# Kernel optimization log

Hardware: AMD Instinct MI355X
Metric: run time of the kernel (lower is better)

The kernel has to match this reference:

```python
import jax, jax.numpy as jnp
import numpy as np

V, E, H, L, C, NH, O, B = 32000, 128, 128, 6, 4, 4, 1024, 16384
HD = H // NH


def setup_inputs() -> dict:
    key = jax.random.key(0)
    ks = jax.random.split(key, 20)
    s = 1.0 / np.sqrt(H).astype(np.float32)

    def rn(k, shape, scale=s):
        return jax.random.normal(k, shape, jnp.float32) * scale

    return {
        "tokens": jax.random.randint(ks[0], (B, 1), 0, V),
        "h": jax.random.normal(ks[1], (L, C, B, H), jnp.float32),
        "emb": rn(ks[2], (V, E), 1.0),
        "wih0_c0": rn(ks[3], (3 * H, E)),
        "wih0_rest": rn(ks[4], (C - 1, 3 * H, 1)),
        "bih0": rn(ks[5], (C, 3 * H)),
        "whh0": rn(ks[6], (C, 3 * H, H)),
        "bhh0": rn(ks[7], (C, 3 * H)),
        "wih": rn(ks[8], (L - 1, C, 3 * H, H)),
        "whh": rn(ks[9], (L - 1, C, 3 * H, H)),
        "bih": rn(ks[10], (L - 1, C, 3 * H)),
        "bhh": rn(ks[11], (L - 1, C, 3 * H)),
        "attn_in_w": rn(ks[12], (L, 3 * H, H)),
        "attn_in_b": rn(ks[13], (L, 3 * H)),
        "attn_out_w": rn(ks[14], (L, H, H), 0.001),  # nn.init.normal_(out_proj.weight, 0, 0.001)
        "attn_out_b": jnp.zeros((L, H), jnp.float32),
        "ln_g": jnp.ones((L, H), jnp.float32),
        "ln_b": jnp.zeros((L, H), jnp.float32),
        "gate_w": rn(ks[15], (L, 2 * H)),
        "gate_b": jnp.zeros((L,), jnp.float32),
        "head_w": rn(ks[16], (O, H)),
        "head_b": jnp.zeros((O,), jnp.float32),
    }


def _gru(gi, gh, h):
    # torch GRUCell: r,z gates sigmoid; n = tanh(in + r*hn); h' = (1-z)*n + z*h
    ir, iz, i_n = jnp.split(gi, 3, -1)
    hr, hz, h_n = jnp.split(gh, 3, -1)
    r = jax.nn.sigmoid(ir + hr)
    z = jax.nn.sigmoid(iz + hz)
    n = jnp.tanh(i_n + r * h_n)
    return (1.0 - z) * n + z * h


def _msg_layer(hn, in_w, in_b, out_w, out_b, g, b):
    # hn: [C,B,H]; MultiheadAttention with batch_first=False (seq=C), then LayerNorm
    qkv = jnp.einsum('cbh,gh->cbg', hn, in_w) + in_b
    q, k, v = jnp.split(qkv, 3, -1)
    q = q.reshape(C, -1, NH, HD)
    k = k.reshape(C, -1, NH, HD)
    v = v.reshape(C, -1, NH, HD)
    scores = jnp.einsum('qbnd,kbnd->bnqk', q, k) / np.sqrt(HD).astype(np.float32)
    a = jax.nn.softmax(scores, axis=-1)
    o = jnp.einsum('bnqk,kbnd->qbnd', a, v).reshape(C, -1, H)
    o = jnp.einsum('cbh,oh->cbo', o, out_w) + out_b
    mu = o.mean(-1, keepdims=True)
    var = o.var(-1, keepdims=True)
    return (o - mu) / jnp.sqrt(var + 1e-5) * g + b


def reference(tokens, h, emb, wih0_c0, wih0_rest, bih0, whh0, bhh0, wih, whh, bih, bhh,
              attn_in_w, attn_in_b, attn_out_w, attn_out_b, ln_g, ln_b,
              gate_w, gate_b, head_w, head_b):
    bsz = tokens.shape[0]
    x0 = emb[tokens[:, 0]]  # [B,E]
    x = None
    h_new = []
    for l in range(L):
        hl = h[l]  # [C,B,H]
        if l == 0:
            gi0 = x0 @ wih0_c0.T + bih0[0]  # col 0 gets the embedding
            # cols 1..C-1 get a zeros(B,1) dummy input -> x @ wih0_rest == 0, bias only
            gi_rest = jnp.broadcast_to(bih0[1:, None, :], (C - 1, bsz, 3 * H))
            gi = jnp.concatenate([gi0[None], gi_rest], 0)
            whh_l, bhh_l = whh0, bhh0
        else:
            gi = jnp.einsum('cbi,cgi->cbg', x, wih[l - 1]) + bih[l - 1][:, None, :]
            whh_l, bhh_l = whh[l - 1], bhh[l - 1]
        gh = jnp.einsum('cbi,cgi->cbg', hl, whh_l) + bhh_l[:, None, :]
        hl_n = _gru(gi, gh, hl)
        msg = _msg_layer(hl_n, attn_in_w[l], attn_in_b[l], attn_out_w[l], attn_out_b[l], ln_g[l], ln_b[l])
        gin = jnp.concatenate([hl_n, msg], -1)  # [C,B,2H]
        gt = jax.nn.sigmoid(jnp.einsum('cbh,h->cb', gin, gate_w[l]) + gate_b[l])[..., None]
        hl_n = (1.0 - gt) * hl_n + gt * msg
        h_new.append(hl_n)
        x = hl_n
    h_n = jnp.stack(h_new, 0)  # [L,C,B,H]
    y = h_n[-1, 0] @ head_w.T + head_b  # head on last layer, column 0
    return (y, h_n)
```

## Files before the change

### kernel.cpp

```cpp
#include <hip/hip_runtime.h>
#include <hip/hip_bf16.h>

#define B_   16384
#define H_   128
#define C_   4
#define L_   6
#define O_   1024
#define G3H  384
#define CB   (C_ * B_)
#define CBH  (C_ * B_ * H_)

typedef __hip_bfloat16 bf16;
using bf16x8  = __attribute__((ext_vector_type(8))) __bf16;
using bf16x4  = __attribute__((ext_vector_type(4))) __bf16;
using floatx4 = __attribute__((ext_vector_type(4))) float;

__device__ __forceinline__ bf16 f2bf(float x) { return __float2bfloat16(x); }
__device__ __forceinline__ float bf2f(bf16 x) { return __bfloat162float(x); }

__device__ __forceinline__ floatx4 mfma16(bf16x8 a, bf16x8 b, floatx4 c) {
  return __builtin_amdgcn_mfma_f32_16x16x32_bf16(a, b, c, 0, 0, 0);
}

__device__ __forceinline__ bf16x8 load8(const bf16* p) { return *(const bf16x8*)p; }
__device__ __forceinline__ bf16x8 load8(const float* p) {
  const float4 a = *(const float4*)p;
  const float4 b = *(const float4*)(p + 4);
  bf16x8 r;
  r[0] = (__bf16)a.x; r[1] = (__bf16)a.y; r[2] = (__bf16)a.z; r[3] = (__bf16)a.w;
  r[4] = (__bf16)b.x; r[5] = (__bf16)b.y; r[6] = (__bf16)b.z; r[7] = (__bf16)b.w;
  return r;
}

__device__ __forceinline__ float sigmoidf_(float x) {
  return 1.f / (1.f + __expf(-x));
}
__device__ __forceinline__ float tanhf_(float x) {
  float e = __expf(2.f * x);
  return 1.f - 2.f / (e + 1.f);
}

struct Cvt7 {
  const float* src[7];
  long start4[8];
};
__global__ __launch_bounds__(256) void cvt7_kernel(Cvt7 a, bf16* __restrict__ dst) {
  long i4 = (long)blockIdx.x * 256 + threadIdx.x;
  if (i4 >= a.start4[7]) return;
  int s = 0;
#pragma unroll
  for (int k = 1; k < 7; ++k)
    if (i4 >= a.start4[k]) s = k;
  const float4 v = ((const float4*)a.src[s])[i4 - a.start4[s]];
  bf16x4 o;
  o[0] = (__bf16)v.x; o[1] = (__bf16)v.y; o[2] = (__bf16)v.z; o[3] = (__bf16)v.w;
  ((bf16x4*)dst)[i4] = o;
}

template <bool L0>
__global__ __launch_bounds__(256) void cell_fused(const float* __restrict__ x,
                                                  const int* __restrict__ tok,
                                                  const float* __restrict__ emb,
                                                  const bf16* __restrict__ wih_l,
                                                  const float* __restrict__ bih_l,
                                                  const float* __restrict__ h,
                                                  const bf16* __restrict__ whh_l,
                                                  const float* __restrict__ bhh_l,
                                                  const bf16* __restrict__ ainw,
                                                  const float* __restrict__ ainb,
                                                  float* __restrict__ hn,
                                                  bf16* __restrict__ qkv) {
  __shared__ __align__(16) char lds[3 * 16384];
  char* h_raw  = lds;
  char* x_raw  = lds + 16384;
  char* hn_raw = lds + 32768;
  char* qkv_raw = lds;

  const int tid = threadIdx.x;
  const int wave = tid >> 6, lane = tid & 63;
  const int sub = lane & 15, quad = lane >> 4;
  const int m0 = blockIdx.x * 64;
  const int cell = m0 / B_;
  const bool has_gi = (!L0) || (cell == 0);

  {
    const int colg = tid & 15;
    const int rb   = tid >> 4;
#pragma unroll
    for (int i = 0; i < 4; ++i) {
      const int row = i * 16 + rb;
      bf16x8 v = load8(h + (long)(m0 + row) * H_ + colg * 8);
      *(bf16x8*)(h_raw + ((row * 256 + colg * 16) ^ ((row & 7) << 4))) = v;
    }
    if (has_gi) {
      if constexpr (L0) {
#pragma unroll
        for (int i = 0; i < 4; ++i) {
          const int row = i * 16 + rb;
          const int tk = tok[m0 + row];
          bf16x8 v = load8(emb + (long)tk * 128 + colg * 8);
          *(bf16x8*)(x_raw + ((row * 256 + colg * 16) ^ ((row & 7) << 4))) = v;
        }
      } else {
#pragma unroll
        for (int i = 0; i < 4; ++i) {
          const int row = i * 16 + rb;
          bf16x8 v = load8(x + (long)(m0 + row) * H_ + colg * 8);
          *(bf16x8*)(x_raw + ((row * 256 + colg * 16) ^ ((row & 7) << 4))) = v;
        }
      }
    }
  }
  __syncthreads();

  const bf16*  Wh = whh_l + (long)cell * G3H * H_;
  const bf16*  Wi = L0 ? wih_l : wih_l + (long)cell * G3H * H_;
  const float* bh = bhh_l + cell * G3H;
  const float* bi = bih_l + cell * G3H;

#pragma unroll
  for (int p = 0; p < 2; ++p) {
    const int colr = wave * 32 + p * 16 + sub;

    bf16x8 wfr[3][4], wif[3][4];
#pragma unroll
    for (int g = 0; g < 3; ++g) {
      const bf16* Wg = Wh + (long)(g * 128 + colr) * H_ + quad * 8;
#pragma unroll
      for (int kc = 0; kc < 4; ++kc) wfr[g][kc] = load8(Wg + kc * 32);
    }
    if (has_gi) {
#pragma unroll
      for (int g = 0; g < 3; ++g) {
        const bf16* Wg = Wi + (long)(g * 128 + colr) * H_ + quad * 8;
#pragma unroll
        for (int kc = 0; kc < 4; ++kc) wif[g][kc] = load8(Wg + kc * 32);
      }
    }

    const float bir = bi[colr],        bhr = bh[colr];
    const float biz = bi[128 + colr],  bhz = bh[128 + colr];
    const float bin_ = bi[256 + colr], bhn = bh[256 + colr];

#pragma unroll
    for (int rt = 0; rt < 4; ++rt) {
      bf16x8 hfr[4];
#pragma unroll
      for (int kc = 0; kc < 4; ++kc) {
        const int lrow = rt * 16 + sub;
        hfr[kc] = *(const bf16x8*)(h_raw +
                   ((lrow * 256 + kc * 64 + quad * 16) ^ ((lrow & 7) << 4)));
      }
      floatx4 ar = {0.f, 0.f, 0.f, 0.f}, az = {0.f, 0.f, 0.f, 0.f};
      floatx4 anh = {0.f, 0.f, 0.f, 0.f}, ani = {0.f, 0.f, 0.f, 0.f};
#pragma unroll
      for (int kc = 0; kc < 4; ++kc) {
        ar  = mfma16(hfr[kc], wfr[0][kc], ar);
        az  = mfma16(hfr[kc], wfr[1][kc], az);
        anh = mfma16(hfr[kc], wfr[2][kc], anh);
      }
      if (has_gi) {
        bf16x8 xfr[4];
#pragma unroll
        for (int kc = 0; kc < 4; ++kc) {
          const int lrow = rt * 16 + sub;
          xfr[kc] = *(const bf16x8*)(x_raw +
                     ((lrow * 256 + kc * 64 + quad * 16) ^ ((lrow & 7) << 4)));
        }
#pragma unroll
        for (int kc = 0; kc < 4; ++kc) {
          ar  = mfma16(xfr[kc], wif[0][kc], ar);
          az  = mfma16(xfr[kc], wif[1][kc], az);
          ani = mfma16(xfr[kc], wif[2][kc], ani);
        }
      }

#pragma unroll
      for (int r = 0; r < 4; ++r) {
        const int lrow = rt * 16 + quad * 4 + r;
        const long grow = m0 + lrow;
        float rg = sigmoidf_(ar[r] + bir + bhr);
        float zg = sigmoidf_(az[r] + biz + bhz);
        float ng = tanhf_(ani[r] + bin_ + rg * (anh[r] + bhn));
        float hv = h[grow * H_ + colr];
        float hnv = (1.f - zg) * ng + zg * hv;
        hn[grow * H_ + colr] = hnv;
        *(bf16*)(hn_raw + ((lrow * 256 + colr * 2) ^ ((lrow & 7) << 4))) = f2bf(hnv);
      }
    }
  }
  __syncthreads();

  bf16x8 af[4][4];
#pragma unroll
  for (int rt = 0; rt < 4; ++rt) {
#pragma unroll
    for (int kc = 0; kc < 4; ++kc) {
      const int lrow = rt * 16 + sub;
      af[rt][kc] = *(const bf16x8*)(hn_raw +
                    ((lrow * 256 + kc * 64 + quad * 16) ^ ((lrow & 7) << 4)));
    }
  }
  __syncthreads();

#pragma unroll
  for (int t = 0; t < 6; ++t) {
    const int col = wave * 96 + t * 16 + sub;
    bf16x8 wf[4];
    const bf16* Wp = ainw + (long)col * H_ + quad * 8;
#pragma unroll
    for (int kc = 0; kc < 4; ++kc) wf[kc] = load8(Wp + kc * 32);
    const float bv = ainb[col];
#pragma unroll
    for (int rt = 0; rt < 4; ++rt) {
      floatx4 acc = {0.f, 0.f, 0.f, 0.f};
#pragma unroll
      for (int kc = 0; kc < 4; ++kc) acc = mfma16(af[rt][kc], wf[kc], acc);
#pragma unroll
      for (int r = 0; r < 4; ++r) {
        const int lrow = rt * 16 + quad * 4 + r;
        *(bf16*)(qkv_raw + ((lrow * 768 + col * 2) ^ ((lrow & 12) << 3))) =
            f2bf(acc[r] + bv);
      }
    }
  }
  __syncthreads();

#pragma unroll
  for (int i = 0; i < 12; ++i) {
    const int m = i * 256 + tid;
    const int row = m / 48, ch = m - row * 48;
    bf16x8 v = *(const bf16x8*)(qkv_raw + ((row * 768 + ch * 16) ^ ((row & 12) << 3)));
    *(bf16x8*)(qkv + (long)(m0 + row) * G3H + ch * 8) = v;
  }
}

__global__ __launch_bounds__(256) void attn_oproj(const bf16* __restrict__ qkv,
                                                  const bf16* __restrict__ w,
                                                  const float* __restrict__ bias,
                                                  const float* __restrict__ g,
                                                  const float* __restrict__ bb,
                                                  const float* __restrict__ gatew,
                                                  const float* __restrict__ gateb,
                                                  float* __restrict__ hn) {
  __shared__ __align__(16) char lds[50176 + 4096 + 16384 + 2048];
  char*  qbase = lds;
  float* p_s   = (float*)(lds + 50176);
  char*  o_raw = lds + 50176 + 4096;
  float* prm   = (float*)(lds + 50176 + 4096 + 16384);
  float* o2_s  = (float*)lds;

  const int tid = threadIdx.x;
  const int wave = tid >> 6, lane = tid & 63;
  const int sub = lane & 15, quad = lane >> 4;
  const int b0 = blockIdx.x * 16;

#pragma unroll
  for (int i = 0; i < 12; ++i) {
    const int idx = i * 256 + tid;
    const int r = idx / 48, ch = idx - r * 48;
    const int c = r >> 4, bj = r & 15;
    bf16x8 v = load8(qkv + ((long)c * B_ + b0 + bj) * G3H + ch * 8);
    *(bf16x8*)(qbase + r * 784 + ch * 16) = v;
  }
  if (tid < 128) {
    prm[tid] = g[tid];
    prm[128 + tid] = bb[tid];
    prm[256 + tid] = gatew[tid];
    prm[384 + tid] = gatew[128 + tid];
  }
  __syncthreads();

  {
    const int hd = wave;
    const int bi = sub >> 2, qc = sub & 3;
    const int bjx = sub >> 2, kc = sub & 3;
#pragma unroll
    for (int bg = 0; bg < 4; ++bg) {
      const int rq = qc * 16 + bg * 4 + bi;
      const int rk = kc * 16 + bg * 4 + bjx;
      bf16x8 qa = *(const bf16x8*)(qbase + rq * 784 + hd * 64 + quad * 16);
      bf16x8 kb = *(const bf16x8*)(qbase + rk * 784 + 256 + hd * 64 + quad * 16);
      floatx4 sc = {0.f, 0.f, 0.f, 0.f};
      sc = mfma16(qa, kb, sc);
      float p[4];
#pragma unroll
      for (int r = 0; r < 4; ++r) {
        float s = sc[r] * 0.17677669529663687f;
        float m = fmaxf(s, __shfl_xor(s, 1));
        m = fmaxf(m, __shfl_xor(m, 2));
        float e = __expf(s - m);
        float ssum = e + __shfl_xor(e, 1);
        ssum += __shfl_xor(ssum, 2);
        p[r] = e / ssum;
      }
      if (quad == bjx) {
        const int bl = bg * 4 + quad;
#pragma unroll
        for (int r = 0; r < 4; ++r)
          p_s[((bl * 4 + hd) * 4 + r) * 4 + kc] = p[r];
      }
    }
  }
  __syncthreads();

#pragma unroll
  for (int i = 0; i < 4; ++i) {
    const int m = i * 256 + tid;
    const int row = m >> 4;
    const int ch = m & 15;
    const int qc = row >> 4, bj = row & 15;
    const int hd = ch >> 2;
    float acc[8];
#pragma unroll
    for (int j = 0; j < 8; ++j) acc[j] = 0.f;
#pragma unroll
    for (int kc = 0; kc < 4; ++kc) {
      const float pv = p_s[((bj * 4 + hd) * 4 + qc) * 4 + kc];
      bf16x8 vv = *(const bf16x8*)(qbase + (kc * 16 + bj) * 784 + 512 + ch * 16);
#pragma unroll
      for (int j = 0; j < 8; ++j) acc[j] += pv * (float)vv[j];
    }
    bf16x8 ov;
#pragma unroll
    for (int j = 0; j < 8; ++j) ov[j] = (__bf16)acc[j];
    *(bf16x8*)(o_raw + ((row * 256 + ch * 16) ^ ((row & 7) << 4))) = ov;
  }
  __syncthreads();

  {
    bf16x8 af[4][4];
#pragma unroll
    for (int rt = 0; rt < 4; ++rt) {
#pragma unroll
      for (int kc = 0; kc < 4; ++kc) {
        const int lrow = rt * 16 + sub;
        af[rt][kc] = *(const bf16x8*)(o_raw +
                      ((lrow * 256 + kc * 64 + quad * 16) ^ ((lrow & 7) << 4)));
      }
    }
#pragma unroll
    for (int p = 0; p < 2; ++p) {
      const int col = wave * 32 + p * 16 + sub;
      bf16x8 wf[4];
      const bf16* Wp = w + (long)col * H_ + quad * 8;
#pragma unroll
      for (int kc = 0; kc < 4; ++kc) wf[kc] = load8(Wp + kc * 32);
      const float bv = bias[col];
#pragma unroll
      for (int rt = 0; rt < 4; ++rt) {
        floatx4 acc = {0.f, 0.f, 0.f, 0.f};
#pragma unroll
        for (int kc = 0; kc < 4; ++kc) acc = mfma16(af[rt][kc], wf[kc], acc);
#pragma unroll
        for (int r = 0; r < 4; ++r)
          o2_s[(rt * 16 + quad * 4 + r) * 132 + col] = acc[r] + bv;
      }
    }
  }
  __syncthreads();

  {
    const int row = tid >> 2;
    const int c0 = (tid & 3) * 32;
    float s = 0.f;
#pragma unroll
    for (int j = 0; j < 32; j += 4) {
      float4 v = *(const float4*)&o2_s[row * 132 + c0 + j];
      s += v.x + v.y + v.z + v.w;
    }
    s += __shfl_xor(s, 1);
    s += __shfl_xor(s, 2);
    const float mu = s * (1.f / 128.f);
    float vs = 0.f;
#pragma unroll
    for (int j = 0; j < 32; j += 4) {
      float4 v = *(const float4*)&o2_s[row * 132 + c0 + j];
      float d0 = v.x - mu, d1 = v.y - mu, d2 = v.z - mu, d3 = v.w - mu;
      vs += d0 * d0 + d1 * d1 + d2 * d2 + d3 * d3;
    }
    vs += __shfl_xor(vs, 1);
    vs += __shfl_xor(vs, 2);
    const float rs = rsqrtf(vs * (1.f / 128.f) + 1e-5f);

    const int qc = row >> 4, bj = row & 15;
    const long grow = (long)qc * B_ + b0 + bj;
    float mv[32], hv[32];
    float gp = 0.f;
#pragma unroll
    for (int j = 0; j < 32; j += 4) {
      float4 v = *(const float4*)&o2_s[row * 132 + c0 + j];
      float4 hh = *(const float4*)&hn[grow * H_ + c0 + j];
      float vv[4] = {v.x, v.y, v.z, v.w};
      float hh4[4] = {hh.x, hh.y, hh.z, hh.w};
#pragma unroll
      for (int q = 0; q < 4; ++q) {
        const int c = c0 + j + q;
        float mval = (vv[q] - mu) * rs * prm[c] + prm[128 + c];
        mv[j + q] = mval;
        hv[j + q] = hh4[q];
        gp += hh4[q] * prm[256 + c] + mval * prm[384 + c];
      }
    }
    gp += __shfl_xor(gp, 1);
    gp += __shfl_xor(gp, 2);
    const float gt = 1.f / (1.f + __expf(-(gp + gateb[0])));
#pragma unroll
    for (int j = 0; j < 32; j += 4) {
      float4 o;
      o.x = (1.f - gt) * hv[j]     + gt * mv[j];
      o.y = (1.f - gt) * hv[j + 1] + gt * mv[j + 1];
      o.z = (1.f - gt) * hv[j + 2] + gt * mv[j + 2];
      o.w = (1.f - gt) * hv[j + 3] + gt * mv[j + 3];
      *(float4*)&hn[grow * H_ + c0 + j] = o;
    }
  }
}

__global__ __launch_bounds__(256) void head_gemm(const float* __restrict__ A,
                                                 const bf16* __restrict__ W,
                                                 const float* __restrict__ bias,
                                                 float* __restrict__ out) {
  __shared__ __align__(16) char a_raw[64 * 256];
  const int tid = threadIdx.x;
  const int wave = tid >> 6, lane = tid & 63;
  const int sub = lane & 15, quad = lane >> 4;
  const int m0 = blockIdx.x * 64;
  const int nb = blockIdx.y * 256;

  {
    const int colg = tid & 15;
    const int rb = tid >> 4;
#pragma unroll
    for (int i = 0; i < 4; ++i) {
      const int row = i * 16 + rb;
      bf16x8 v = load8(A + (long)(m0 + row) * H_ + colg * 8);
      *(bf16x8*)(a_raw + ((row * 256 + colg * 16) ^ ((row & 7) << 4))) = v;
    }
  }
  __syncthreads();

  bf16x8 af[4][4];
#pragma unroll
  for (int rt = 0; rt < 4; ++rt) {
#pragma unroll
    for (int kc = 0; kc < 4; ++kc) {
      const int lrow = rt * 16 + sub;
      af[rt][kc] = *(const bf16x8*)(a_raw +
                    ((lrow * 256 + kc * 64 + quad * 16) ^ ((lrow & 7) << 4)));
    }
  }
#pragma unroll
  for (int ct = 0; ct < 4; ++ct) {
    const int col = nb + wave * 64 + ct * 16 + sub;
    bf16x8 wf[4];
    const bf16* Wp = W + (long)col * H_ + quad * 8;
#pragma unroll
    for (int kc = 0; kc < 4; ++kc) wf[kc] = load8(Wp + kc * 32);
    const float bv = bias[col];
#pragma unroll
    for (int rt = 0; rt < 4; ++rt) {
      floatx4 acc = {0.f, 0.f, 0.f, 0.f};
#pragma unroll
      for (int kc = 0; kc < 4; ++kc) acc = mfma16(af[rt][kc], wf[kc], acc);
#pragma unroll
      for (int r = 0; r < 4; ++r)
        out[(long)(m0 + rt * 16 + quad * 4 + r) * O_ + col] = acc[r] + bv;
    }
  }
}

extern "C" void kernel_launch(void* const* d_in, const int* in_sizes, int n_in,
                              void* d_out, int out_size, void* d_ws, size_t ws_size,
                              hipStream_t stream) {
  const int*   tokens = (const int*)d_in[0];
  const float* h      = (const float*)d_in[1];
  const float* emb    = (const float*)d_in[2];
  const float* wih0c0 = (const float*)d_in[3];
  const float* bih0   = (const float*)d_in[5];
  const float* whh0   = (const float*)d_in[6];
  const float* bhh0   = (const float*)d_in[7];
  const float* wih    = (const float*)d_in[8];
  const float* whh    = (const float*)d_in[9];
  const float* bih    = (const float*)d_in[10];
  const float* bhh    = (const float*)d_in[11];
  const float* ainw   = (const float*)d_in[12];
  const float* ainb   = (const float*)d_in[13];
  const float* aoutw  = (const float*)d_in[14];
  const float* aoutb  = (const float*)d_in[15];
  const float* lng    = (const float*)d_in[16];
  const float* lnb    = (const float*)d_in[17];
  const float* gw     = (const float*)d_in[18];
  const float* gb     = (const float*)d_in[19];
  const float* headw  = (const float*)d_in[20];
  const float* headb  = (const float*)d_in[21];

  float* y_out  = (float*)d_out;
  float* hn_out = (float*)d_out + (long)B_ * O_;

  bf16* ws = (bf16*)d_ws;
  bf16* bufA = ws;
  bf16* wp   = bufA + (long)CB * G3H;
  bf16* wih0bf  = wp;                  wp += 49152;
  bf16* whh0bf  = wp;                  wp += 196608;
  bf16* wihbf   = wp;                  wp += 983040;
  bf16* whhbf   = wp;                  wp += 983040;
  bf16* ainwbf  = wp;                  wp += 294912;
  bf16* aoutwbf = wp;                  wp += 98304;
  bf16* headwbf = wp;                  wp += 131072;

  dim3 blk(256);

  {
    Cvt7 a;
    const float* srcs[7] = {wih0c0, whh0, wih, whh, ainw, aoutw, headw};
    const long lens[7] = {49152, 196608, 983040, 983040, 294912, 98304, 131072};
    long cum = 0;
    for (int i = 0; i < 7; ++i) { a.src[i] = srcs[i]; a.start4[i] = cum / 4; cum += lens[i]; }
    a.start4[7] = cum / 4;
    const long n4 = cum / 4;
    cvt7_kernel<<<(int)((n4 + 255) / 256), blk, 0, stream>>>(a, wih0bf);
  }

  for (int l = 0; l < L_; ++l) {
    float* hn_l = hn_out + (long)l * CBH;
    const float* hl = h + (long)l * CBH;

    if (l == 0) {
      cell_fused<true><<<CB / 64, blk, 0, stream>>>(
          nullptr, tokens, emb, wih0bf, bih0, hl, whh0bf, bhh0,
          ainwbf, ainb, hn_l, bufA);
    } else {
      cell_fused<false><<<CB / 64, blk, 0, stream>>>(
          hn_out + (long)(l - 1) * CBH, nullptr, nullptr,
          wihbf + (long)(l - 1) * C_ * G3H * H_, bih + (long)(l - 1) * C_ * G3H,
          hl, whhbf + (long)(l - 1) * C_ * G3H * H_, bhh + (long)(l - 1) * C_ * G3H,
          ainwbf + (long)l * G3H * H_, ainb + (long)l * G3H, hn_l, bufA);
    }

    attn_oproj<<<B_ / 16, blk, 0, stream>>>(
        bufA, aoutwbf + (long)l * H_ * H_, aoutb + (long)l * H_,
        lng + l * H_, lnb + l * H_, gw + l * 2 * H_, gb + l, hn_l);
  }

  head_gemm<<<dim3(B_ / 64, O_ / 256), blk, 0, stream>>>(
      hn_out + (long)5 * CBH, headwbf, headb, y_out);
}
```

Baseline: 1.074 ms.

## Fuse all layers, attention and head into one persistent per-batch-tile kernel

Replaces the per-layer cell_fused, attn_oproj and head_gemm launches with a single kernel where each block owns 16 batch rows across all 4 columns and all 6 layers. Hidden state, QKV and the next-layer input stay in LDS and registers, which removes the bf16 QKV workspace round trip and the re-read of hn between kernels and layers. The cost is that each block now reloads every layer's weights for only 16 rows per column, so MFMA tiles per weight load shrink and weight traffic through L2 grows. The launch bound also drops to 2 blocks per CU, and the head GEMM now covers all 1024 outputs per block.

```diff
diff --git a/kernel.cpp b/kernel.cpp
--- a/kernel.cpp
+++ b/kernel.cpp
@@ -57,415 +57,346 @@
   ((bf16x4*)dst)[i4] = o;
 }
 
-template <bool L0>
-__global__ __launch_bounds__(256) void cell_fused(const float* __restrict__ x,
-                                                  const int* __restrict__ tok,
-                                                  const float* __restrict__ emb,
-                                                  const bf16* __restrict__ wih_l,
-                                                  const float* __restrict__ bih_l,
-                                                  const float* __restrict__ h,
-                                                  const bf16* __restrict__ whh_l,
-                                                  const float* __restrict__ bhh_l,
-                                                  const bf16* __restrict__ ainw,
-                                                  const float* __restrict__ ainb,
-                                                  float* __restrict__ hn,
-                                                  bf16* __restrict__ qkv) {
-  __shared__ __align__(16) char lds[3 * 16384];
-  char* h_raw  = lds;
-  char* x_raw  = lds + 16384;
-  char* hn_raw = lds + 32768;
-  char* qkv_raw = lds;
+struct P {
+  const int* tok; const float* h; const float* emb;
+  const bf16 *wih0, *whh0, *wih, *whh, *ainw, *aoutw, *headw;
+  const float *bih0, *bhh0, *bih, *bhh, *ainb, *aoutb, *lng, *lnb, *gw, *gb, *headb;
+  float *y, *hn;
+};
+
+__global__ __launch_bounds__(256, 2) void gridrnn(P p) {
+  __shared__ __align__(16) char D[49152];
+  __shared__ __align__(16) char X[16384];
+  __shared__ __align__(16) float p_s[1024];
 
   const int tid = threadIdx.x;
   const int wave = tid >> 6, lane = tid & 63;
   const int sub = lane & 15, quad = lane >> 4;
-  const int m0 = blockIdx.x * 64;
-  const int cell = m0 / B_;
-  const bool has_gi = (!L0) || (cell == 0);
+  const int b0 = blockIdx.x * 16;
 
   {
-    const int colg = tid & 15;
-    const int rb   = tid >> 4;
+    const int row = tid >> 4, ch = tid & 15;
+    const int tk = p.tok[b0 + row];
+    bf16x8 v = load8(p.emb + (long)tk * 128 + ch * 8);
+    *(bf16x8*)(X + ((row * 256 + ch * 16) ^ ((row & 7) << 4))) = v;
+  }
+
+  float hnreg[8][4];
+
+#pragma unroll 1
+  for (int l = 0; l < L_; ++l) {
+    __syncthreads();
+    const float* hl = p.h + (long)l * CBH;
 #pragma unroll
     for (int i = 0; i < 4; ++i) {
-      const int row = i * 16 + rb;
-      bf16x8 v = load8(h + (long)(m0 + row) * H_ + colg * 8);
-      *(bf16x8*)(h_raw + ((row * 256 + colg * 16) ^ ((row & 7) << 4))) = v;
-    }
+      const int idx = i * 256 + tid;
+      const int row = idx >> 4, ch = idx & 15;
+      const long grow = (long)(row >> 4) * B_ + b0 + (row & 15);
+      bf16x8 v = load8(hl + grow * H_ + ch * 8);
+      *(bf16x8*)(D + ((row * 256 + ch * 16) ^ ((row & 7) << 4))) = v;
+    }
+    __syncthreads();
+
+    const bool has_gi = (l > 0) || (wave == 0);
+    const bf16* Wh = (l == 0 ? p.whh0 : p.whh + (long)(l - 1) * C_ * G3H * H_) +
+                     (long)wave * G3H * H_;
+    const bf16* Wi = (l == 0)
+                         ? p.wih0
+                         : p.wih + (long)(l - 1) * C_ * G3H * H_ + (long)wave * G3H * H_;
+    const float* bh = (l == 0 ? p.bhh0 : p.bhh + (long)(l - 1) * C_ * G3H) + wave * G3H;
+    const float* bi = (l == 0 ? p.bih0 : p.bih + (long)(l - 1) * C_ * G3H) + wave * G3H;
+
+    const int arow = wave * 16 + sub;
+    bf16x8 hfr[4], xfr[4];
+#pragma unroll
+    for (int kc = 0; kc < 4; ++kc)
+      hfr[kc] = *(const bf16x8*)(D + ((arow * 256 + kc * 64 + quad * 16) ^
+                                      ((arow & 7) << 4)));
     if (has_gi) {
-      if constexpr (L0) {
-#pragma unroll
-        for (int i = 0; i < 4; ++i) {
-          const int row = i * 16 + rb;
-          const int tk = tok[m0 + row];
-          bf16x8 v = load8(emb + (long)tk * 128 + colg * 8);
-          *(bf16x8*)(x_raw + ((row * 256 + colg * 16) ^ ((row & 7) << 4))) = v;
-        }
-      } else {
-#pragma unroll
-        for (int i = 0; i < 4; ++i) {
-          const int row = i * 16 + rb;
-          bf16x8 v = load8(x + (long)(m0 + row) * H_ + colg * 8);
-          *(bf16x8*)(x_raw + ((row * 256 + colg * 16) ^ ((row & 7) << 4))) = v;
-        }
-      }
-    }
-  }
-  __syncthreads();
-
-  const bf16*  Wh = whh_l + (long)cell * G3H * H_;
-  const bf16*  Wi = L0 ? wih_l : wih_l + (long)cell * G3H * H_;
-  const float* bh = bhh_l + cell * G3H;
-  const float* bi = bih_l + cell * G3H;
-
-#pragma unroll
-  for (int p = 0; p < 2; ++p) {
-    const int colr = wave * 32 + p * 16 + sub;
-
-    bf16x8 wfr[3][4], wif[3][4];
-#pragma unroll
-    for (int g = 0; g < 3; ++g) {
-      const bf16* Wg = Wh + (long)(g * 128 + colr) * H_ + quad * 8;
-#pragma unroll
-      for (int kc = 0; kc < 4; ++kc) wfr[g][kc] = load8(Wg + kc * 32);
-    }
-    if (has_gi) {
+#pragma unroll
+      for (int kc = 0; kc < 4; ++kc)
+        xfr[kc] = *(const bf16x8*)(X + ((arow * 256 + kc * 64 + quad * 16) ^
+                                        ((arow & 7) << 4)));
+    }
+
+#pragma unroll
+    for (int pp = 0; pp < 8; ++pp) {
+      const int colr = pp * 16 + sub;
+      bf16x8 wfr[3][4];
 #pragma unroll
       for (int g = 0; g < 3; ++g) {
-        const bf16* Wg = Wi + (long)(g * 128 + colr) * H_ + quad * 8;
-#pragma unroll
-        for (int kc = 0; kc < 4; ++kc) wif[g][kc] = load8(Wg + kc * 32);
-      }
-    }
-
-    const float bir = bi[colr],        bhr = bh[colr];
-    const float biz = bi[128 + colr],  bhz = bh[128 + colr];
-    const float bin_ = bi[256 + colr], bhn = bh[256 + colr];
-
-#pragma unroll
-    for (int rt = 0; rt < 4; ++rt) {
-      bf16x8 hfr[4];
-#pragma unroll
-      for (int kc = 0; kc < 4; ++kc) {
-        const int lrow = rt * 16 + sub;
-        hfr[kc] = *(const bf16x8*)(h_raw +
-                   ((lrow * 256 + kc * 64 + quad * 16) ^ ((lrow & 7) << 4)));
+        const bf16* Wg = Wh + (long)(g * 128 + colr) * H_ + quad * 8;
+#pragma unroll
+        for (int kc = 0; kc < 4; ++kc) wfr[g][kc] = load8(Wg + kc * 32);
       }
       floatx4 ar = {0.f, 0.f, 0.f, 0.f}, az = {0.f, 0.f, 0.f, 0.f};
       floatx4 anh = {0.f, 0.f, 0.f, 0.f}, ani = {0.f, 0.f, 0.f, 0.f};
+      if (has_gi) {
+        bf16x8 wif[3][4];
+#pragma unroll
+        for (int g = 0; g < 3; ++g) {
+          const bf16* Wg = Wi + (long)(g * 128 + colr) * H_ + quad * 8;
+#pragma unroll
+          for (int kc = 0; kc < 4; ++kc) wif[g][kc] = load8(Wg + kc * 32);
+        }
+#pragma unroll
+        for (int kc = 0; kc < 4; ++kc) {
+          ar  = mfma16(xfr[kc], wif[0][kc], ar);
+          az  = mfma16(xfr[kc], wif[1][kc], az);
+          ani = mfma16(xfr[kc], wif[2][kc], ani);
+        }
+      }
 #pragma unroll
       for (int kc = 0; kc < 4; ++kc) {
         ar  = mfma16(hfr[kc], wfr[0][kc], ar);
         az  = mfma16(hfr[kc], wfr[1][kc], az);
         anh = mfma16(hfr[kc], wfr[2][kc], anh);
       }
-      if (has_gi) {
-        bf16x8 xfr[4];
-#pragma unroll
-        for (int kc = 0; kc < 4; ++kc) {
-          const int lrow = rt * 16 + sub;
-          xfr[kc] = *(const bf16x8*)(x_raw +
-                     ((lrow * 256 + kc * 64 + quad * 16) ^ ((lrow & 7) << 4)));
-        }
-#pragma unroll
-        for (int kc = 0; kc < 4; ++kc) {
-          ar  = mfma16(xfr[kc], wif[0][kc], ar);
-          az  = mfma16(xfr[kc], wif[1][kc], az);
-          ani = mfma16(xfr[kc], wif[2][kc], ani);
-        }
-      }
-
+
+      const float bir = bi[colr],        bhr = bh[colr];
+      const float biz = bi[128 + colr],  bhz = bh[128 + colr];
+      const float bin_ = bi[256 + colr], bhn = bh[256 + colr];
 #pragma unroll
       for (int r = 0; r < 4; ++r) {
-        const int lrow = rt * 16 + quad * 4 + r;
-        const long grow = m0 + lrow;
+        const int lrow = wave * 16 + quad * 4 + r;
+        const long grow = (long)wave * B_ + b0 + quad * 4 + r;
         float rg = sigmoidf_(ar[r] + bir + bhr);
         float zg = sigmoidf_(az[r] + biz + bhz);
         float ng = tanhf_(ani[r] + bin_ + rg * (anh[r] + bhn));
-        float hv = h[grow * H_ + colr];
+        float hv = hl[grow * H_ + colr];
         float hnv = (1.f - zg) * ng + zg * hv;
-        hn[grow * H_ + colr] = hnv;
-        *(bf16*)(hn_raw + ((lrow * 256 + colr * 2) ^ ((lrow & 7) << 4))) = f2bf(hnv);
-      }
-    }
-  }
-  __syncthreads();
-
-  bf16x8 af[4][4];
-#pragma unroll
-  for (int rt = 0; rt < 4; ++rt) {
-#pragma unroll
-    for (int kc = 0; kc < 4; ++kc) {
-      const int lrow = rt * 16 + sub;
-      af[rt][kc] = *(const bf16x8*)(hn_raw +
-                    ((lrow * 256 + kc * 64 + quad * 16) ^ ((lrow & 7) << 4)));
-    }
-  }
-  __syncthreads();
-
-#pragma unroll
-  for (int t = 0; t < 6; ++t) {
-    const int col = wave * 96 + t * 16 + sub;
-    bf16x8 wf[4];
-    const bf16* Wp = ainw + (long)col * H_ + quad * 8;
-#pragma unroll
-    for (int kc = 0; kc < 4; ++kc) wf[kc] = load8(Wp + kc * 32);
-    const float bv = ainb[col];
-#pragma unroll
-    for (int rt = 0; rt < 4; ++rt) {
-      floatx4 acc = {0.f, 0.f, 0.f, 0.f};
-#pragma unroll
-      for (int kc = 0; kc < 4; ++kc) acc = mfma16(af[rt][kc], wf[kc], acc);
-#pragma unroll
-      for (int r = 0; r < 4; ++r) {
-        const int lrow = rt * 16 + quad * 4 + r;
-        *(bf16*)(qkv_raw + ((lrow * 768 + col * 2) ^ ((lrow & 12) << 3))) =
-            f2bf(acc[r] + bv);
-      }
-    }
-  }
-  __syncthreads();
-
-#pragma unroll
-  for (int i = 0; i < 12; ++i) {
-    const int m = i * 256 + tid;
-    const int row = m / 48, ch = m - row * 48;
-    bf16x8 v = *(const bf16x8*)(qkv_raw + ((row * 768 + ch * 16) ^ ((row & 12) << 3)));
-    *(bf16x8*)(qkv + (long)(m0 + row) * G3H + ch * 8) = v;
-  }
-}
-
-__global__ __launch_bounds__(256) void attn_oproj(const bf16* __restrict__ qkv,
-                                                  const bf16* __restrict__ w,
-                                                  const float* __restrict__ bias,
-                                                  const float* __restrict__ g,
-                                                  const float* __restrict__ bb,
-                                                  const float* __restrict__ gatew,
-                                                  const float* __restrict__ gateb,
-                                                  float* __restrict__ hn) {
-  __shared__ __align__(16) char lds[50176 + 4096 + 16384 + 2048];
-  char*  qbase = lds;
-  float* p_s   = (float*)(lds + 50176);
-  char*  o_raw = lds + 50176 + 4096;
-  float* prm   = (float*)(lds + 50176 + 4096 + 16384);
-  float* o2_s  = (float*)lds;
-
-  const int tid = threadIdx.x;
-  const int wave = tid >> 6, lane = tid & 63;
-  const int sub = lane & 15, quad = lane >> 4;
-  const int b0 = blockIdx.x * 16;
-
-#pragma unroll
-  for (int i = 0; i < 12; ++i) {
-    const int idx = i * 256 + tid;
-    const int r = idx / 48, ch = idx - r * 48;
-    const int c = r >> 4, bj = r & 15;
-    bf16x8 v = load8(qkv + ((long)c * B_ + b0 + bj) * G3H + ch * 8);
-    *(bf16x8*)(qbase + r * 784 + ch * 16) = v;
-  }
-  if (tid < 128) {
-    prm[tid] = g[tid];
-    prm[128 + tid] = bb[tid];
-    prm[256 + tid] = gatew[tid];
-    prm[384 + tid] = gatew[128 + tid];
-  }
-  __syncthreads();
-
-  {
-    const int hd = wave;
-    const int bi = sub >> 2, qc = sub & 3;
-    const int bjx = sub >> 2, kc = sub & 3;
-#pragma unroll
-    for (int bg = 0; bg < 4; ++bg) {
-      const int rq = qc * 16 + bg * 4 + bi;
-      const int rk = kc * 16 + bg * 4 + bjx;
-      bf16x8 qa = *(const bf16x8*)(qbase + rq * 784 + hd * 64 + quad * 16);
-      bf16x8 kb = *(const bf16x8*)(qbase + rk * 784 + 256 + hd * 64 + quad * 16);
-      floatx4 sc = {0.f, 0.f, 0.f, 0.f};
-      sc = mfma16(qa, kb, sc);
-      float p[4];
-#pragma unroll
-      for (int r = 0; r < 4; ++r) {
-        float s = sc[r] * 0.17677669529663687f;
-        float m = fmaxf(s, __shfl_xor(s, 1));
-        m = fmaxf(m, __shfl_xor(m, 2));
-        float e = __expf(s - m);
-        float ssum = e + __shfl_xor(e, 1);
-        ssum += __shfl_xor(ssum, 2);
-        p[r] = e / ssum;
-      }
-      if (quad == bjx) {
-        const int bl = bg * 4 + quad;
-#pragma unroll
-        for (int r = 0; r < 4; ++r)
-          p_s[((bl * 4 + hd) * 4 + r) * 4 + kc] = p[r];
-      }
-    }
-  }
-  __syncthreads();
-
-#pragma unroll
-  for (int i = 0; i < 4; ++i) {
-    const int m = i * 256 + tid;
-    const int row = m >> 4;
-    const int ch = m & 15;
-    const int qc = row >> 4, bj = row & 15;
-    const int hd = ch >> 2;
-    float acc[8];
-#pragma unroll
-    for (int j = 0; j < 8; ++j) acc[j] = 0.f;
-#pragma unroll
-    for (int kc = 0; kc < 4; ++kc) {
-      const float pv = p_s[((bj * 4 + hd) * 4 + qc) * 4 + kc];
-      bf16x8 vv = *(const bf16x8*)(qbase + (kc * 16 + bj) * 784 + 512 + ch * 16);
-#pragma unroll
-      for (int j = 0; j < 8; ++j) acc[j] += pv * (float)vv[j];
-    }
-    bf16x8 ov;
-#pragma unroll
-    for (int j = 0; j < 8; ++j) ov[j] = (__bf16)acc[j];
-    *(bf16x8*)(o_raw + ((row * 256 + ch * 16) ^ ((row & 7) << 4))) = ov;
-  }
-  __syncthreads();
-
-  {
+        hnreg[pp][r] = hnv;
+        *(bf16*)(D + 16384 + ((lrow * 256 + colr * 2) ^ ((lrow & 7) << 4))) = f2bf(hnv);
+      }
+    }
+    __syncthreads();
+
     bf16x8 af[4][4];
 #pragma unroll
-    for (int rt = 0; rt < 4; ++rt) {
+    for (int rt = 0; rt < 4; ++rt)
 #pragma unroll
       for (int kc = 0; kc < 4; ++kc) {
         const int lrow = rt * 16 + sub;
-        af[rt][kc] = *(const bf16x8*)(o_raw +
+        af[rt][kc] = *(const bf16x8*)(D + 16384 +
                       ((lrow * 256 + kc * 64 + quad * 16) ^ ((lrow & 7) << 4)));
       }
-    }
-#pragma unroll
-    for (int p = 0; p < 2; ++p) {
-      const int col = wave * 32 + p * 16 + sub;
+    __syncthreads();
+
+    {
+      const bf16* ainw_l = p.ainw + (long)l * G3H * H_;
+      const float* ainb_l = p.ainb + (long)l * G3H;
+#pragma unroll
+      for (int t = 0; t < 6; ++t) {
+        const int col = wave * 96 + t * 16 + sub;
+        const bf16* Wp = ainw_l + (long)col * H_ + quad * 8;
+        bf16x8 wf[4];
+#pragma unroll
+        for (int kc = 0; kc < 4; ++kc) wf[kc] = load8(Wp + kc * 32);
+        const float bv = ainb_l[col];
+        const int tile = (col >> 7) * 16384;
+        const int lcol = col & 127;
+#pragma unroll
+        for (int rt = 0; rt < 4; ++rt) {
+          floatx4 acc = {0.f, 0.f, 0.f, 0.f};
+#pragma unroll
+          for (int kc = 0; kc < 4; ++kc) acc = mfma16(af[rt][kc], wf[kc], acc);
+#pragma unroll
+          for (int r = 0; r < 4; ++r) {
+            const int lrow = rt * 16 + quad * 4 + r;
+            *(bf16*)(D + tile + ((lrow * 256 + lcol * 2) ^ ((lrow & 7) << 4))) =
+                f2bf(acc[r] + bv);
+          }
+        }
+      }
+    }
+    __syncthreads();
+
+    {
+      const int hd = wave;
+#pragma unroll
+      for (int bg = 0; bg < 4; ++bg) {
+        const int rr = (sub & 3) * 16 + bg * 4 + (sub >> 2);
+        const int soff = ((rr * 256 + hd * 64 + quad * 16) ^ ((rr & 7) << 4));
+        bf16x8 qa = *(const bf16x8*)(D + soff);
+        bf16x8 kb = *(const bf16x8*)(D + 16384 + soff);
+        floatx4 sc = {0.f, 0.f, 0.f, 0.f};
+        sc = mfma16(qa, kb, sc);
+        float pr[4];
+#pragma unroll
+        for (int r = 0; r < 4; ++r) {
+          float s = sc[r] * 0.17677669529663687f;
+          float m = fmaxf(s, __shfl_xor(s, 1));
+          m = fmaxf(m, __shfl_xor(m, 2));
+          float e = __expf(s - m);
+          float ss = e + __shfl_xor(e, 1);
+          ss += __shfl_xor(ss, 2);
+          pr[r] = e / ss;
+        }
+        if (quad == (sub >> 2)) {
+          const int bl = bg * 4 + quad;
+#pragma unroll
+          for (int r = 0; r < 4; ++r)
+            p_s[((bl * 4 + hd) * 4 + r) * 4 + (sub & 3)] = pr[r];
+        }
+      }
+    }
+    __syncthreads();
+
+#pragma unroll
+    for (int i = 0; i < 4; ++i) {
+      const int m = i * 256 + tid;
+      const int row = m >> 4, ch = m & 15;
+      const int qc = row >> 4, bj = row & 15, hd = ch >> 2;
+      float acc[8];
+#pragma unroll
+      for (int j = 0; j < 8; ++j) acc[j] = 0.f;
+#pragma unroll
+      for (int kc = 0; kc < 4; ++kc) {
+        const float pv = p_s[((bj * 4 + hd) * 4 + qc) * 4 + kc];
+        const int vrow = kc * 16 + bj;
+        bf16x8 vv = *(const bf16x8*)(D + 32768 +
+                     ((vrow * 256 + ch * 16) ^ ((vrow & 7) << 4)));
+#pragma unroll
+        for (int j = 0; j < 8; ++j) acc[j] += pv * (float)vv[j];
+      }
+      bf16x8 ov;
+#pragma unroll
+      for (int j = 0; j < 8; ++j) ov[j] = (__bf16)acc[j];
+      *(bf16x8*)(D + ((row * 256 + ch * 16) ^ ((row & 7) << 4))) = ov;
+    }
+    __syncthreads();
+
+    bf16x8 af2[4][4];
+#pragma unroll
+    for (int rt = 0; rt < 4; ++rt)
+#pragma unroll
+      for (int kc = 0; kc < 4; ++kc) {
+        const int lrow = rt * 16 + sub;
+        af2[rt][kc] = *(const bf16x8*)(D +
+                       ((lrow * 256 + kc * 64 + quad * 16) ^ ((lrow & 7) << 4)));
+      }
+    __syncthreads();
+
+    float* o2 = (float*)D;
+    {
+      const bf16* aoutw_l = p.aoutw + (long)l * H_ * H_;
+      const float* aoutb_l = p.aoutb + (long)l * H_;
+#pragma unroll
+      for (int p2 = 0; p2 < 2; ++p2) {
+        const int col = wave * 32 + p2 * 16 + sub;
+        const bf16* Wp = aoutw_l + (long)col * H_ + quad * 8;
+        bf16x8 wf[4];
+#pragma unroll
+        for (int kc = 0; kc < 4; ++kc) wf[kc] = load8(Wp + kc * 32);
+        const float bv = aoutb_l[col];
+#pragma unroll
+        for (int rt = 0; rt < 4; ++rt) {
+          floatx4 acc = {0.f, 0.f, 0.f, 0.f};
+#pragma unroll
+          for (int kc = 0; kc < 4; ++kc) acc = mfma16(af2[rt][kc], wf[kc], acc);
+#pragma unroll
+          for (int r = 0; r < 4; ++r)
+            o2[(rt * 16 + quad * 4 + r) * 132 + col] = acc[r] + bv;
+        }
+      }
+    }
+    __syncthreads();
+
+    {
+      float o2v[8][4];
+#pragma unroll
+      for (int pi = 0; pi < 8; ++pi)
+#pragma unroll
+        for (int r = 0; r < 4; ++r)
+          o2v[pi][r] = o2[(wave * 16 + quad * 4 + r) * 132 + pi * 16 + sub];
+
+      float mu[4], rs[4];
+#pragma unroll
+      for (int r = 0; r < 4; ++r) {
+        float s = 0.f;
+#pragma unroll
+        for (int pi = 0; pi < 8; ++pi) s += o2v[pi][r];
+        s += __shfl_xor(s, 1); s += __shfl_xor(s, 2);
+        s += __shfl_xor(s, 4); s += __shfl_xor(s, 8);
+        mu[r] = s * (1.f / 128.f);
+      }
+#pragma unroll
+      for (int r = 0; r < 4; ++r) {
+        float vs = 0.f;
+#pragma unroll
+        for (int pi = 0; pi < 8; ++pi) {
+          float d = o2v[pi][r] - mu[r];
+          vs += d * d;
+        }
+        vs += __shfl_xor(vs, 1); vs += __shfl_xor(vs, 2);
+        vs += __shfl_xor(vs, 4); vs += __shfl_xor(vs, 8);
+        rs[r] = rsqrtf(vs * (1.f / 128.f) + 1e-5f);
+      }
+
+      const float* lngl = p.lng + l * H_;
+      const float* lnbl = p.lnb + l * H_;
+      const float* gwl  = p.gw + l * 2 * H_;
+      float msg[8][4];
+      float gpp[4] = {0.f, 0.f, 0.f, 0.f};
+#pragma unroll
+      for (int pi = 0; pi < 8; ++pi) {
+        const int c = pi * 16 + sub;
+        const float gv = lngl[c], bv2 = lnbl[c];
+        const float g1 = gwl[c], g2 = gwl[128 + c];
+#pragma unroll
+        for (int r = 0; r < 4; ++r) {
+          float mval = (o2v[pi][r] - mu[r]) * rs[r] * gv + bv2;
+          msg[pi][r] = mval;
+          gpp[r] += hnreg[pi][r] * g1 + mval * g2;
+        }
+      }
+      const float gbl = p.gb[l];
+      float gt[4];
+#pragma unroll
+      for (int r = 0; r < 4; ++r) {
+        float s = gpp[r];
+        s += __shfl_xor(s, 1); s += __shfl_xor(s, 2);
+        s += __shfl_xor(s, 4); s += __shfl_xor(s, 8);
+        gt[r] = sigmoidf_(s + gbl);
+      }
+      float* hnl = p.hn + (long)l * CBH;
+#pragma unroll
+      for (int pi = 0; pi < 8; ++pi) {
+        const int c = pi * 16 + sub;
+#pragma unroll
+        for (int r = 0; r < 4; ++r) {
+          const int lrow = wave * 16 + quad * 4 + r;
+          const long grow = (long)wave * B_ + b0 + quad * 4 + r;
+          float outv = (1.f - gt[r]) * hnreg[pi][r] + gt[r] * msg[pi][r];
+          hnl[grow * H_ + c] = outv;
+          *(bf16*)(X + ((lrow * 256 + c * 2) ^ ((lrow & 7) << 4))) = f2bf(outv);
+        }
+      }
+    }
+  }
+
+  __syncthreads();
+
+  {
+    bf16x8 afh[4];
+#pragma unroll
+    for (int kc = 0; kc < 4; ++kc)
+      afh[kc] = *(const bf16x8*)(X + ((sub * 256 + kc * 64 + quad * 16) ^
+                                      ((sub & 7) << 4)));
+#pragma unroll
+    for (int t = 0; t < 16; ++t) {
+      const int col = wave * 256 + t * 16 + sub;
+      const bf16* Wp = p.headw + (long)col * H_ + quad * 8;
       bf16x8 wf[4];
-      const bf16* Wp = w + (long)col * H_ + quad * 8;
 #pragma unroll
       for (int kc = 0; kc < 4; ++kc) wf[kc] = load8(Wp + kc * 32);
-      const float bv = bias[col];
-#pragma unroll
-      for (int rt = 0; rt < 4; ++rt) {
-        floatx4 acc = {0.f, 0.f, 0.f, 0.f};
-#pragma unroll
-        for (int kc = 0; kc < 4; ++kc) acc = mfma16(af[rt][kc], wf[kc], acc);
-#pragma unroll
-        for (int r = 0; r < 4; ++r)
-          o2_s[(rt * 16 + quad * 4 + r) * 132 + col] = acc[r] + bv;
-      }
-    }
-  }
-  __syncthreads();
-
-  {
-    const int row = tid >> 2;
-    const int c0 = (tid & 3) * 32;
-    float s = 0.f;
-#pragma unroll
-    for (int j = 0; j < 32; j += 4) {
-      float4 v = *(const float4*)&o2_s[row * 132 + c0 + j];
-      s += v.x + v.y + v.z + v.w;
-    }
-    s += __shfl_xor(s, 1);
-    s += __shfl_xor(s, 2);
-    const float mu = s * (1.f / 128.f);
-    float vs = 0.f;
-#pragma unroll
-    for (int j = 0; j < 32; j += 4) {
-      float4 v = *(const float4*)&o2_s[row * 132 + c0 + j];
-      float d0 = v.x - mu, d1 = v.y - mu, d2 = v.z - mu, d3 = v.w - mu;
-      vs += d0 * d0 + d1 * d1 + d2 * d2 + d3 * d3;
-    }
-    vs += __shfl_xor(vs, 1);
-    vs += __shfl_xor(vs, 2);
-    const float rs = rsqrtf(vs * (1.f / 128.f) + 1e-5f);
-
-    const int qc = row >> 4, bj = row & 15;
-    const long grow = (long)qc * B_ + b0 + bj;
-    float mv[32], hv[32];
-    float gp = 0.f;
-#pragma unroll
-    for (int j = 0; j < 32; j += 4) {
-      float4 v = *(const float4*)&o2_s[row * 132 + c0 + j];
-      float4 hh = *(const float4*)&hn[grow * H_ + c0 + j];
-      float vv[4] = {v.x, v.y, v.z, v.w};
-      float hh4[4] = {hh.x, hh.y, hh.z, hh.w};
-#pragma unroll
-      for (int q = 0; q < 4; ++q) {
-        const int c = c0 + j + q;
-        float mval = (vv[q] - mu) * rs * prm[c] + prm[128 + c];
-        mv[j + q] = mval;
-        hv[j + q] = hh4[q];
-        gp += hh4[q] * prm[256 + c] + mval * prm[384 + c];
-      }
-    }
-    gp += __shfl_xor(gp, 1);
-    gp += __shfl_xor(gp, 2);
-    const float gt = 1.f / (1.f + __expf(-(gp + gateb[0])));
-#pragma unroll
-    for (int j = 0; j < 32; j += 4) {
-      float4 o;
-      o.x = (1.f - gt) * hv[j]     + gt * mv[j];
-      o.y = (1.f - gt) * hv[j + 1] + gt * mv[j + 1];
-      o.z = (1.f - gt) * hv[j + 2] + gt * mv[j + 2];
-      o.w = (1.f - gt) * hv[j + 3] + gt * mv[j + 3];
-      *(float4*)&hn[grow * H_ + c0 + j] = o;
-    }
-  }
-}
-
-__global__ __launch_bounds__(256) void head_gemm(const float* __restrict__ A,
-                                                 const bf16* __restrict__ W,
-                                                 const float* __restrict__ bias,
-                                                 float* __restrict__ out) {
-  __shared__ __align__(16) char a_raw[64 * 256];
-  const int tid = threadIdx.x;
-  const int wave = tid >> 6, lane = tid & 63;
-  const int sub = lane & 15, quad = lane >> 4;
-  const int m0 = blockIdx.x * 64;
-  const int nb = blockIdx.y * 256;
-
-  {
-    const int colg = tid & 15;
-    const int rb = tid >> 4;
-#pragma unroll
-    for (int i = 0; i < 4; ++i) {
-      const int row = i * 16 + rb;
-      bf16x8 v = load8(A + (long)(m0 + row) * H_ + colg * 8);
-      *(bf16x8*)(a_raw + ((row * 256 + colg * 16) ^ ((row & 7) << 4))) = v;
-    }
-  }
-  __syncthreads();
-
-  bf16x8 af[4][4];
-#pragma unroll
-  for (int rt = 0; rt < 4; ++rt) {
-#pragma unroll
-    for (int kc = 0; kc < 4; ++kc) {
-      const int lrow = rt * 16 + sub;
-      af[rt][kc] = *(const bf16x8*)(a_raw +
-                    ((lrow * 256 + kc * 64 + quad * 16) ^ ((lrow & 7) << 4)));
-    }
-  }
-#pragma unroll
-  for (int ct = 0; ct < 4; ++ct) {
-    const int col = nb + wave * 64 + ct * 16 + sub;
-    bf16x8 wf[4];
-    const bf16* Wp = W + (long)col * H_ + quad * 8;
-#pragma unroll
-    for (int kc = 0; kc < 4; ++kc) wf[kc] = load8(Wp + kc * 32);
-    const float bv = bias[col];
-#pragma unroll
-    for (int rt = 0; rt < 4; ++rt) {
+      const float bv = p.headb[col];
       floatx4 acc = {0.f, 0.f, 0.f, 0.f};
 #pragma unroll
-      for (int kc = 0; kc < 4; ++kc) acc = mfma16(af[rt][kc], wf[kc], acc);
+      for (int kc = 0; kc < 4; ++kc) acc = mfma16(afh[kc], wf[kc], acc);
 #pragma unroll
       for (int r = 0; r < 4; ++r)
-        out[(long)(m0 + rt * 16 + quad * 4 + r) * O_ + col] = acc[r] + bv;
+        p.y[(long)(b0 + quad * 4 + r) * O_ + col] = acc[r] + bv;
     }
   }
 }
@@ -498,9 +429,7 @@
   float* y_out  = (float*)d_out;
   float* hn_out = (float*)d_out + (long)B_ * O_;
 
-  bf16* ws = (bf16*)d_ws;
-  bf16* bufA = ws;
-  bf16* wp   = bufA + (long)CB * G3H;
+  bf16* wp = (bf16*)d_ws;
   bf16* wih0bf  = wp;                  wp += 49152;
   bf16* whh0bf  = wp;                  wp += 196608;
   bf16* wihbf   = wp;                  wp += 983040;
@@ -510,7 +439,6 @@
   bf16* headwbf = wp;                  wp += 131072;
 
   dim3 blk(256);
-
   {
     Cvt7 a;
     const float* srcs[7] = {wih0c0, whh0, wih, whh, ainw, aoutw, headw};
@@ -522,27 +450,14 @@
     cvt7_kernel<<<(int)((n4 + 255) / 256), blk, 0, stream>>>(a, wih0bf);
   }
 
-  for (int l = 0; l < L_; ++l) {
-    float* hn_l = hn_out + (long)l * CBH;
-    const float* hl = h + (long)l * CBH;
-
-    if (l == 0) {
-      cell_fused<true><<<CB / 64, blk, 0, stream>>>(
-          nullptr, tokens, emb, wih0bf, bih0, hl, whh0bf, bhh0,
-          ainwbf, ainb, hn_l, bufA);
-    } else {
-      cell_fused<false><<<CB / 64, blk, 0, stream>>>(
-          hn_out + (long)(l - 1) * CBH, nullptr, nullptr,
-          wihbf + (long)(l - 1) * C_ * G3H * H_, bih + (long)(l - 1) * C_ * G3H,
-          hl, whhbf + (long)(l - 1) * C_ * G3H * H_, bhh + (long)(l - 1) * C_ * G3H,
-          ainwbf + (long)l * G3H * H_, ainb + (long)l * G3H, hn_l, bufA);
-    }
-
-    attn_oproj<<<B_ / 16, blk, 0, stream>>>(
-        bufA, aoutwbf + (long)l * H_ * H_, aoutb + (long)l * H_,
-        lng + l * H_, lnb + l * H_, gw + l * 2 * H_, gb + l, hn_l);
-  }
-
-  head_gemm<<<dim3(B_ / 64, O_ / 256), blk, 0, stream>>>(
-      hn_out + (long)5 * CBH, headwbf, headb, y_out);
-}
+  P pp;
+  pp.tok = tokens; pp.h = h; pp.emb = emb;
+  pp.wih0 = wih0bf; pp.whh0 = whh0bf; pp.wih = wihbf; pp.whh = whhbf;
+  pp.ainw = ainwbf; pp.aoutw = aoutwbf; pp.headw = headwbf;
+  pp.bih0 = bih0; pp.bhh0 = bhh0; pp.bih = bih; pp.bhh = bhh;
+  pp.ainb = ainb; pp.aoutb = aoutb; pp.lng = lng; pp.lnb = lnb;
+  pp.gw = gw; pp.gb = gb; pp.headb = headb;
+  pp.y = y_out; pp.hn = hn_out;
+
+  gridrnn<<<B_ / 16, blk, 0, stream>>>(pp);
+}
```

After: 1.451 ms. +35.2%, slower.
